# Kernel optimization log

Hardware: AMD Instinct MI355X
Metric: run time of the kernel (lower is better)

## Reference

```python
import jax, jax.numpy as jnp
import numpy as np
from jax import lax

# idx_match from the torch code: five 13-wide segments of the 64 features
# (note segments 0 and 1 overlap at feature index 12, exactly as in the source).
IDX = jnp.asarray(np.stack([np.arange(0, 13), np.arange(12, 25), np.arange(25, 38),
                            np.arange(38, 51), np.arange(51, 64)]))  # (5, 13) int

N, C, F, D = 375, 5, 64, 13


def setup_inputs() -> dict:
    key = jax.random.key(0)
    ks = jax.random.split(key, 6)
    inp = {"picture": jax.random.normal(ks[0], (N, C, F), dtype=jnp.float32)}
    for i in range(5):
        inp[f"token{i}"] = jax.random.normal(ks[i + 1], (D,), dtype=jnp.float32)
    return inp


def _greedy_assign(Dmat):
    """Greedy bipartite matching on a (5,5) cost matrix.
    Repeatedly take the global argmin, record (class_row -> token_col),
    and exclude that row and column. Returns assign[class_row] = token_col."""
    INF = jnp.asarray(1e30, Dmat.dtype)
    rows = jnp.arange(5)

    def step(carry, _):
        mask, assign = carry  # mask: (5,5) bool availability
        flat = jnp.argmin(jnp.where(mask, Dmat, INF))
        r = flat // 5
        c = flat % 5
        assign = assign.at[r].set(c.astype(jnp.int32))
        mask = mask & (rows[:, None] != r) & (rows[None, :] != c)
        return (mask, assign), None

    init = (jnp.ones((5, 5), dtype=bool), jnp.zeros(5, dtype=jnp.int32))
    (_, assign), _ = lax.scan(step, init, None, length=5)
    return assign


def reference(picture, token0, token1, token2, token3, token4):
    T = jnp.stack([token0, token1, token2, token3, token4])  # (5, 13)
    # seg[i, j, k, :] = picture[i, j, idx_match[k]]
    seg = picture[:, :, IDX]                                  # (375, 5, 5, 13)
    full_sq = jnp.sum(picture * picture, axis=-1)             # (375, 5)
    diff = seg - T[None, None]                                # (375, 5, 5, 13)
    # distance_absolute0[j,k] = ||pic_j||^2 - ||pic_j[idx_k]||^2 + ||pic_j[idx_k] - token_k||^2
    Dmat = (full_sq[:, :, None]
            - jnp.sum(seg * seg, axis=-1)
            + jnp.sum(diff * diff, axis=-1))                  # (375, 5, 5)

    assign = jax.vmap(_greedy_assign)(Dmat)                   # (375, 5): token idx per class row
    gathered = T[assign]                                      # (375, 5, 13)

    # scatter: support_token[i, class_r, idx_match[class_r]] += token[assign[class_r]]
    bi = jnp.arange(N)[:, None, None]                         # (375,1,1)
    ri = jnp.arange(5)[None, :, None]                         # (1,5,1)
    out = jnp.zeros((N, C, F), dtype=picture.dtype)
    out = out.at[bi, ri, IDX[None]].add(gathered)
    return out
```

## Files before the change

kernel.cpp:

```cpp
#include <hip/hip_runtime.h>


__global__ __launch_bounds__(64) void token_kernel(
    const float* __restrict__ picture,
    const float* __restrict__ t0, const float* __restrict__ t1,
    const float* __restrict__ t2, const float* __restrict__ t3,
    const float* __restrict__ t4,
    float* __restrict__ out)
{
    const int n = blockIdx.x;
    const int t = threadIdx.x;

    __shared__ float T[5][13];
    __shared__ float pic[5][64];
    __shared__ float Dm[5][5];
    __shared__ float fullsq[5];
    __shared__ int   assign[5];

    const float* toks[5] = {t0, t1, t2, t3, t4};
    for (int i = t; i < 65; i += 64) {
        int s = i / 13, j = i % 13;
        T[s][j] = toks[s][j];
    }

    const float* p = picture + n * 320;
    float v[5];
#pragma unroll
    for (int c = 0; c < 5; ++c) {
        v[c] = p[c * 64 + t];
        pic[c][t] = v[c];
    }

#pragma unroll
    for (int c = 0; c < 5; ++c) {
        float s = v[c] * v[c];
#pragma unroll
        for (int off = 32; off > 0; off >>= 1)
            s += __shfl_down(s, off, 64);
        if (t == 0) fullsq[c] = s;
    }
    __syncthreads();

    if (t < 25) {
        int c = t / 5, s = t % 5;
        int start = (s == 0) ? 0 : (s == 1) ? 12 : (s == 2) ? 25 : (s == 3) ? 38 : 51;
        float segsq = 0.f, diffsq = 0.f;
        for (int j = 0; j < 13; ++j) {
            float x = pic[c][start + j];
            float d = x - T[s][j];
            segsq  += x * x;
            diffsq += d * d;
        }
        Dm[c][s] = (fullsq[c] - segsq) + diffsq;
    }
    __syncthreads();

    if (t == 0) {
        bool rm[5] = {true, true, true, true, true};
        bool cm[5] = {true, true, true, true, true};
        for (int it = 0; it < 5; ++it) {
            float best = 1e30f;
            int br = 0, bc = 0;
            for (int r = 0; r < 5; ++r) {
                if (!rm[r]) continue;
                for (int c = 0; c < 5; ++c) {
                    if (!cm[c]) continue;
                    float val = Dm[r][c];
                    if (val < best) { best = val; br = r; bc = c; }
                }
            }
            assign[br] = bc;
            rm[br] = false;
            cm[bc] = false;
        }
    }
    __syncthreads();

    float* o = out + n * 320;
    const int starts[5] = {0, 12, 25, 38, 51};
#pragma unroll
    for (int r = 0; r < 5; ++r) {
        int j = t - starts[r];
        float val = (j >= 0 && j < 13) ? T[assign[r]][j] : 0.f;
        o[r * 64 + t] = val;
    }
}

extern "C" void kernel_launch(void* const* d_in, const int* in_sizes, int n_in,
                              void* d_out, int out_size, void* d_ws, size_t ws_size,
                              hipStream_t stream) {
    const float* picture = (const float*)d_in[0];
    token_kernel<<<dim3(375), dim3(64), 0, stream>>>(
        picture,
        (const float*)d_in[1], (const float*)d_in[2], (const float*)d_in[3],
        (const float*)d_in[4], (const float*)d_in[5],
        (float*)d_out);
}
```

Before: 66.55 us.

## Replace serial greedy matching with wave-shuffle argmin and drop block barriers

```diff
diff --git a/kernel.cpp b/kernel.cpp
--- a/kernel.cpp
+++ b/kernel.cpp
@@ -13,15 +13,13 @@
 
     __shared__ float T[5][13];
     __shared__ float pic[5][64];
-    __shared__ float Dm[5][5];
-    __shared__ float fullsq[5];
-    __shared__ int   assign[5];
 
-    const float* toks[5] = {t0, t1, t2, t3, t4};
-    for (int i = t; i < 65; i += 64) {
-        int s = i / 13, j = i % 13;
-        T[s][j] = toks[s][j];
-    }
+    if (t < 13)      T[0][t]      = t0[t];
+    else if (t < 26) T[1][t - 13] = t1[t - 13];
+    else if (t < 39) T[2][t - 26] = t2[t - 26];
+    else if (t < 52) T[3][t - 39] = t3[t - 39];
+    else             T[4][t - 52] = t4[t - 52];
+    if (t == 0)      T[4][12]     = t4[12];
 
     const float* p = picture + n * 320;
     float v[5];
@@ -31,57 +29,60 @@
         pic[c][t] = v[c];
     }
 
+    const int row = t / 5;
+    const int col = t % 5;
+
+    float myfullsq = 0.f;
 #pragma unroll
     for (int c = 0; c < 5; ++c) {
         float s = v[c] * v[c];
 #pragma unroll
         for (int off = 32; off > 0; off >>= 1)
             s += __shfl_down(s, off, 64);
-        if (t == 0) fullsq[c] = s;
+        float tot = __shfl(s, 0, 64);
+        if (row == c) myfullsq = tot;
     }
+
     __syncthreads();
 
+    const int starts[5] = {0, 12, 25, 38, 51};
+    float dval = 1e30f;
     if (t < 25) {
-        int c = t / 5, s = t % 5;
-        int start = (s == 0) ? 0 : (s == 1) ? 12 : (s == 2) ? 25 : (s == 3) ? 38 : 51;
+        const int start = starts[col];
         float segsq = 0.f, diffsq = 0.f;
         for (int j = 0; j < 13; ++j) {
-            float x = pic[c][start + j];
-            float d = x - T[s][j];
+            float x = pic[row][start + j];
+            float d = x - T[col][j];
             segsq  += x * x;
             diffsq += d * d;
         }
-        Dm[c][s] = (fullsq[c] - segsq) + diffsq;
+        dval = (myfullsq - segsq) + diffsq;
     }
-    __syncthreads();
 
-    if (t == 0) {
-        bool rm[5] = {true, true, true, true, true};
-        bool cm[5] = {true, true, true, true, true};
-        for (int it = 0; it < 5; ++it) {
-            float best = 1e30f;
-            int br = 0, bc = 0;
-            for (int r = 0; r < 5; ++r) {
-                if (!rm[r]) continue;
-                for (int c = 0; c < 5; ++c) {
-                    if (!cm[c]) continue;
-                    float val = Dm[r][c];
-                    if (val < best) { best = val; br = r; bc = c; }
-                }
-            }
-            assign[br] = bc;
-            rm[br] = false;
-            cm[bc] = false;
+    bool alive = (t < 25);
+    int my_assign = 0;
+#pragma unroll
+    for (int it = 0; it < 5; ++it) {
+        float mval = alive ? dval : 1e30f;
+        int   midx = t;
+#pragma unroll
+        for (int off = 16; off > 0; off >>= 1) {
+            float ov = __shfl_down(mval, off, 64);
+            int   oi = __shfl_down(midx, off, 64);
+            if (ov < mval || (ov == mval && oi < midx)) { mval = ov; midx = oi; }
         }
+        const int widx = __shfl(midx, 0, 64);
+        const int br = widx / 5, bc = widx % 5;
+        if (row == br || col == bc) alive = false;
+        if (t == br) my_assign = bc;
     }
-    __syncthreads();
 
     float* o = out + n * 320;
-    const int starts[5] = {0, 12, 25, 38, 51};
 #pragma unroll
     for (int r = 0; r < 5; ++r) {
-        int j = t - starts[r];
-        float val = (j >= 0 && j < 13) ? T[assign[r]][j] : 0.f;
+        const int ar = __shfl(my_assign, r, 64);
+        const int j = t - starts[r];
+        const float val = (j >= 0 && j < 13) ? T[ar][j] : 0.f;
         o[r * 64 + t] = val;
     }
 }
```

Measured after the change: 66.64 us. Within noise of the previous version (+0.1%).
